# Optimization experiments

Hardware: AMD Instinct MI355X
Metric: run time of the kernel (lower is better)

## Reference

```python
import jax, jax.numpy as jnp
import numpy as np

EMA_OLD = 0.01  # original: m[z] = m[z]*0.01 + y*0.99
EMA_NEW = 0.99

def setup_inputs() -> dict:
    key = jax.random.key(0)
    k1, k2, k3, k4 = jax.random.split(key, 4)
    B, n, C, L = 4096, 1024, 64, 64
    y = jax.random.normal(k1, (B, C, L), dtype=jnp.float32)   # encoder latents
    m = jax.random.normal(k2, (n, C, L), dtype=jnp.float32)   # codebook means
    sd = jax.random.uniform(k3, (n, C, L), dtype=jnp.float32) # codebook variances (init ones in orig)
    p = jax.random.uniform(k4, (n,), dtype=jnp.float32)       # cluster counts
    return {"y": y, "m": m, "sd": sd, "p": p}

def reference(y, m, sd, p):
    B, C, L = y.shape
    n = m.shape[0]
    # pairwise squared distances via ||y||^2 - 2 y.m + ||m||^2 (GEMM form)
    yf = y.reshape(B, C * L)
    mf = m.reshape(n, C * L)
    d2 = ((yf * yf).sum(-1, keepdims=True)
          - 2.0 * (yf @ mf.T)
          + (mf * mf).sum(-1)[None, :])            # [B, n]
    z = jnp.argmin(d2, axis=1)                      # [B] assignments
    new_m = m.at[z].set(m[z] * EMA_OLD + y * EMA_NEW)
    # original updates sd using the ALREADY-updated m gathered at z
    mg = new_m[z]
    new_sd = sd.at[z].set((mg - y) ** 2 * EMA_OLD + sd[z] * EMA_NEW)
    return jnp.concatenate([new_m, new_sd], axis=0)  # [2n, C, L]
```

## Files before the change

kernel.cpp:

```cpp
#include <hip/hip_runtime.h>

#define B_ROWS 4096
#define N_CLUST 1024
#define KDIM 4096
#define NKT 32

#define EMA_OLD 0.01f
#define EMA_NEW 0.99f
#define MARGIN 2.0f

typedef unsigned short ushortT;
typedef _Float16 half8 __attribute__((ext_vector_type(8)));
typedef float f32x16 __attribute__((ext_vector_type(16)));

#define WS_WINNER_OFF 0
#define WS_Z_OFF      4096
#define WS_YY_OFF     20480
#define WS_MM_OFF     36864
#define WS_D2A_OFF    65536
#define WS_D2B_OFF    (WS_D2A_OFF + 16777216)
#define WS_YHI_OFF    (WS_D2B_OFF + 16777216)
#define WS_MHI_OFF    (WS_YHI_OFF + 33554432)
#define WS_END        (WS_MHI_OFF + 8388608)

__global__ __launch_bounds__(256) void convert_sumsq(
    const float* __restrict__ ysrc, const float* __restrict__ msrc,
    ushortT* __restrict__ yhi, ushortT* __restrict__ mhi,
    float* __restrict__ yy, float* __restrict__ mm) {
    const int blk = blockIdx.x;
    const float* src;
    ushortT* hi;
    float* out;
    int row;
    if (blk < B_ROWS) {
        src = ysrc; hi = yhi; out = yy + blk; row = blk;
    } else {
        row = blk - B_ROWS;
        src = msrc; hi = mhi; out = mm + row;
    }
    const int r = row & 63, rb = row >> 6;
    const int t = threadIdx.x;
    float s = 0.f;
#pragma unroll
    for (int h = 0; h < 2; ++h) {
        int ci = h * 256 + t;
        int kt = ci >> 4, p = ci & 15;
        int c = p ^ (r & 15);
        const float* sp = src + ((size_t)row << 12) + kt * 128 + c * 8;
        float4 v0 = *(const float4*)sp;
        float4 v1 = *(const float4*)(sp + 4);
        float vv[8] = {v0.x, v0.y, v0.z, v0.w, v1.x, v1.y, v1.z, v1.w};
        half8 hv;
#pragma unroll
        for (int i = 0; i < 8; ++i) {
            hv[i] = (_Float16)vv[i];
            s += vv[i] * vv[i];
        }
        size_t off = (((size_t)rb * NKT + kt) * 64 + r) * 128 + p * 8;
        *(half8*)(hi + off) = hv;
    }
    for (int off = 32; off > 0; off >>= 1) s += __shfl_down(s, off, 64);
    __shared__ float red[4];
    if ((t & 63) == 0) red[t >> 6] = s;
    __syncthreads();
    if (t == 0) out[0] = red[0] + red[1] + red[2] + red[3];
}

__device__ __forceinline__ void gload_lds16(const void* g, void* l) {
    __builtin_amdgcn_global_load_lds(
        (const __attribute__((address_space(1))) unsigned int*)g,
        (__attribute__((address_space(3))) unsigned int*)l, 16, 0, 0);
}

__device__ __forceinline__ half8 ldfrag(const ushortT* s, int r, int c) {
    int p = c ^ (r & 15);
    return *(const half8*)(s + r * 128 + p * 8);
}

__global__ __launch_bounds__(256, 2) void screen_gemm(
    const ushortT* __restrict__ Ah, const ushortT* __restrict__ Bh,
    const float* __restrict__ yy, const float* __restrict__ mm,
    float* __restrict__ d2a, float* __restrict__ d2b) {
    __shared__ __align__(16) ushortT sA[128 * 128];
    __shared__ __align__(16) ushortT sB[128 * 128];

    const int t = threadIdx.x, w = t >> 6, l = t & 63;
    const int by = blockIdx.x & 7;
    const int kh = (blockIdx.x >> 3) & 1;
    const int bx = blockIdx.x >> 4;
    const int row0 = bx * 128, col0 = by * 128;
    const int wr = (w >> 1) * 64, wc = (w & 1) * 64;
    const int m0 = l & 31, hsel = l >> 5;

    const char* gAbase = (const char*)Ah + (size_t)l * 16;
    const char* gBbase = (const char*)Bh + (size_t)l * 16;

    f32x16 acc[2][2];
#pragma unroll
    for (int i = 0; i < 2; ++i)
#pragma unroll
        for (int j = 0; j < 2; ++j)
#pragma unroll
            for (int r = 0; r < 16; ++r) acc[i][j][r] = 0.f;

    const int kt0 = kh * (NKT / 2);
    for (int ktt = 0; ktt < NKT / 2; ++ktt) {
        const int kt = kt0 + ktt;
        __syncthreads();
#pragma unroll
        for (int j = 0; j < 8; ++j) {
            int ch = w * 8 + j;
            int tile = ch >> 4, seg = ch & 15;
            size_t go = ((size_t)((2 * bx + tile) * NKT + kt) << 14) +
                        seg * 1024;
            gload_lds16(gAbase + go, (char*)sA + tile * 16384 + seg * 1024);
            size_t gob = ((size_t)((2 * by + tile) * NKT + kt) << 14) +
                         seg * 1024;
            gload_lds16(gBbase + gob, (char*)sB + tile * 16384 + seg * 1024);
        }
        __syncthreads();

        const ushortT* tA = sA + (wr >> 6) * 8192;
        const ushortT* tB = sB + (wc >> 6) * 8192;
#pragma unroll
        for (int kk = 0; kk < 8; ++kk) {
            int c = kk * 2 + hsel;
            half8 a0 = ldfrag(tA, m0, c);
            half8 a1 = ldfrag(tA, 32 + m0, c);
            half8 b0 = ldfrag(tB, m0, c);
            half8 b1 = ldfrag(tB, 32 + m0, c);
            acc[0][0] = __builtin_amdgcn_mfma_f32_32x32x16_f16(a0, b0, acc[0][0], 0, 0, 0);
            acc[0][1] = __builtin_amdgcn_mfma_f32_32x32x16_f16(a0, b1, acc[0][1], 0, 0, 0);
            acc[1][0] = __builtin_amdgcn_mfma_f32_32x32x16_f16(a1, b0, acc[1][0], 0, 0, 0);
            acc[1][1] = __builtin_amdgcn_mfma_f32_32x32x16_f16(a1, b1, acc[1][1], 0, 0, 0);
        }
    }

    if (kh == 0) {
#pragma unroll
        for (int i = 0; i < 2; ++i)
#pragma unroll
            for (int j = 0; j < 2; ++j) {
                const int gcol = col0 + wc + j * 32 + m0;
                const float mv = mm[gcol];
#pragma unroll
                for (int r = 0; r < 16; ++r) {
                    int ri = (r & 3) + 8 * (r >> 2) + 4 * hsel;
                    int grow = row0 + wr + i * 32 + ri;
                    d2a[(size_t)grow * N_CLUST + gcol] =
                        yy[grow] - 2.0f * acc[i][j][r] + mv;
                }
            }
    } else {
#pragma unroll
        for (int i = 0; i < 2; ++i)
#pragma unroll
            for (int j = 0; j < 2; ++j) {
                const int gcol = col0 + wc + j * 32 + m0;
#pragma unroll
                for (int r = 0; r < 16; ++r) {
                    int ri = (r & 3) + 8 * (r >> 2) + 4 * hsel;
                    int grow = row0 + wr + i * 32 + ri;
                    d2b[(size_t)grow * N_CLUST + gcol] = -2.0f * acc[i][j][r];
                }
            }
    }
}

__global__ __launch_bounds__(256) void rescreen(
    const float* __restrict__ d2a, const float* __restrict__ d2b,
    const float* __restrict__ ysrc, const float* __restrict__ msrc,
    const float* __restrict__ yy, const float* __restrict__ mm,
    int* __restrict__ z) {
    const int row = blockIdx.x * 4 + (threadIdx.x >> 6);
    const int l = threadIdx.x & 63;
    const float* dra = d2a + (size_t)row * N_CLUST;
    const float* drb = d2b + (size_t)row * N_CLUST;

    float v[16];
#pragma unroll
    for (int k = 0; k < 16; ++k) v[k] = dra[l + 64 * k] + drb[l + 64 * k];

    float mn = v[0];
#pragma unroll
    for (int k = 1; k < 16; ++k) mn = fminf(mn, v[k]);
#pragma unroll
    for (int s = 1; s <= 32; s <<= 1) mn = fminf(mn, __shfl_xor(mn, s, 64));
    const float thr = mn + MARGIN;

    int cnt = 0;
#pragma unroll
    for (int k = 0; k < 16; ++k) cnt += (v[k] <= thr) ? 1 : 0;
#pragma unroll
    for (int s = 1; s <= 32; s <<= 1) cnt += __shfl_xor(cnt, s, 64);

    int zj;
    if (cnt == 1) {
        int cj = 0x7FFFFFFF;
#pragma unroll
        for (int k = 0; k < 16; ++k)
            if (v[k] <= thr) cj = min(cj, l + 64 * k);
#pragma unroll
        for (int s = 1; s <= 32; s <<= 1) cj = min(cj, __shfl_xor(cj, s, 64));
        zj = cj;
    } else {
        double bestd = 1e300;
        int bestj = -1;
        const float4* yp = (const float4*)(ysrc + (size_t)row * KDIM);
        for (int k = 0; k < 16; ++k) {
            unsigned long long mask = __ballot(v[k] <= thr);
            while (mask) {
                int lb = __ffsll((unsigned long long)mask) - 1;
                mask &= mask - 1;
                int j = 64 * k + lb;
                const float4* mp = (const float4*)(msrc + (size_t)j * KDIM);
                double acc = 0.0;
#pragma unroll
                for (int tt = 0; tt < 16; ++tt) {
                    float4 a = yp[l + 64 * tt];
                    float4 b = mp[l + 64 * tt];
                    acc += (double)a.x * b.x + (double)a.y * b.y +
                           (double)a.z * b.z + (double)a.w * b.w;
                }
#pragma unroll
                for (int s = 1; s <= 32; s <<= 1)
                    acc += __shfl_xor(acc, s, 64);
                double d2x = (double)yy[row] - 2.0 * acc + (double)mm[j];
                if (d2x < bestd) { bestd = d2x; bestj = j; }
            }
        }
        zj = bestj;
    }
    if (l == 0) z[row] = zj;
}

__global__ void pick_winner(const int* __restrict__ z,
                            int* __restrict__ winner) {
    int b = blockIdx.x * blockDim.x + threadIdx.x;
    if (b < B_ROWS) atomicMax(&winner[z[b]], b);
}

__global__ __launch_bounds__(256) void write_out(
    const float* __restrict__ y, const float* __restrict__ m,
    const float* __restrict__ sd, const int* __restrict__ winner,
    float* __restrict__ out) {
    const int idx = blockIdx.x;
    const int t = threadIdx.x;
    const int w = winner[idx];
    const float4* mp = (const float4*)(m + (size_t)idx * KDIM);
    const float4* sp = (const float4*)(sd + (size_t)idx * KDIM);
    float4* om = (float4*)(out + (size_t)idx * KDIM);
    float4* os = (float4*)(out + (size_t)(N_CLUST + idx) * KDIM);
    if (w >= 0) {
        const float4* yp = (const float4*)(y + (size_t)w * KDIM);
        for (int i = t; i < KDIM / 4; i += 256) {
            float4 mv = mp[i], yv = yp[i], sv = sp[i];
            float4 nm, ns;
            nm.x = mv.x * EMA_OLD + yv.x * EMA_NEW;
            nm.y = mv.y * EMA_OLD + yv.y * EMA_NEW;
            nm.z = mv.z * EMA_OLD + yv.z * EMA_NEW;
            nm.w = mv.w * EMA_OLD + yv.w * EMA_NEW;
            float dx = nm.x - yv.x, dy = nm.y - yv.y;
            float dz = nm.z - yv.z, dw = nm.w - yv.w;
            ns.x = dx * dx * EMA_OLD + sv.x * EMA_NEW;
            ns.y = dy * dy * EMA_OLD + sv.y * EMA_NEW;
            ns.z = dz * dz * EMA_OLD + sv.z * EMA_NEW;
            ns.w = dw * dw * EMA_OLD + sv.w * EMA_NEW;
            om[i] = nm;
            os[i] = ns;
        }
    } else {
        for (int i = t; i < KDIM / 4; i += 256) {
            om[i] = mp[i];
            os[i] = sp[i];
        }
    }
}

extern "C" void kernel_launch(void* const* d_in, const int* in_sizes, int n_in,
                              void* d_out, int out_size, void* d_ws,
                              size_t ws_size, hipStream_t stream) {
    const float* y  = (const float*)d_in[0];
    const float* m  = (const float*)d_in[1];
    const float* sd = (const float*)d_in[2];
    float* out = (float*)d_out;

    char* ws = (char*)d_ws;
    int* winner = (int*)(ws + WS_WINNER_OFF);
    int* z      = (int*)(ws + WS_Z_OFF);
    float* yy   = (float*)(ws + WS_YY_OFF);
    float* mm   = (float*)(ws + WS_MM_OFF);
    float* d2a  = (float*)(ws + WS_D2A_OFF);
    float* d2b  = (float*)(ws + WS_D2B_OFF);
    ushortT* yhi = (ushortT*)(ws + WS_YHI_OFF);
    ushortT* mhi = (ushortT*)(ws + WS_MHI_OFF);

    hipMemsetAsync(winner, 0xFF, 4096, stream);

    convert_sumsq<<<B_ROWS + N_CLUST, 256, 0, stream>>>(y, m, yhi, mhi, yy, mm);

    screen_gemm<<<(B_ROWS / 128) * (N_CLUST / 128) * 2, 256, 0, stream>>>(
        yhi, mhi, yy, mm, d2a, d2b);

    rescreen<<<B_ROWS / 4, 256, 0, stream>>>(d2a, d2b, y, m, yy, mm, z);

    pick_winner<<<B_ROWS / 256, 256, 0, stream>>>(z, winner);
    write_out<<<N_CLUST, 256, 0, stream>>>(y, m, sd, winner, out);
}
```

Baseline: 216.3 us.

## Double-buffer screen GEMM with half-width K tiles and async LDS prefetch

Splits each 128-wide K tile into two 64-wide halves and double-buffers them in LDS. The next stage is prefetched with global_load_lds while the current stage runs MFMA, using s_waitcnt vmcnt and raw barriers in place of two __syncthreads per tile. It also raises wave priority around the MFMA block. LDS footprint stays the same, but there are twice as many loop iterations and barriers, and correctness depends on the manual vmcnt count and the new swizzle and lane offsets.

Result: slower. 222.6 us (+2.9%).

```diff
diff --git a/kernel.cpp b/kernel.cpp
--- a/kernel.cpp
+++ b/kernel.cpp
@@ -4,6 +4,7 @@
 #define N_CLUST 1024
 #define KDIM 4096
 #define NKT 32
+#define NSTEP 32
 
 #define EMA_OLD 0.01f
 #define EMA_NEW 0.99f
@@ -72,17 +73,17 @@
         (__attribute__((address_space(3))) unsigned int*)l, 16, 0, 0);
 }
 
-__device__ __forceinline__ half8 ldfrag(const ushortT* s, int r, int c) {
-    int p = c ^ (r & 15);
-    return *(const half8*)(s + r * 128 + p * 8);
+__device__ __forceinline__ half8 ldfrag64(const ushortT* s, int r, int c) {
+    int p = c ^ (r & 7);
+    return *(const half8*)(s + r * 64 + p * 8);
 }
 
 __global__ __launch_bounds__(256, 2) void screen_gemm(
     const ushortT* __restrict__ Ah, const ushortT* __restrict__ Bh,
     const float* __restrict__ yy, const float* __restrict__ mm,
     float* __restrict__ d2a, float* __restrict__ d2b) {
-    __shared__ __align__(16) ushortT sA[128 * 128];
-    __shared__ __align__(16) ushortT sB[128 * 128];
+    __shared__ __align__(16) ushortT sA[2][128 * 64];
+    __shared__ __align__(16) ushortT sB[2][128 * 64];
 
     const int t = threadIdx.x, w = t >> 6, l = t & 63;
     const int by = blockIdx.x & 7;
@@ -92,8 +93,9 @@
     const int wr = (w >> 1) * 64, wc = (w & 1) * 64;
     const int m0 = l & 31, hsel = l >> 5;
 
-    const char* gAbase = (const char*)Ah + (size_t)l * 16;
-    const char* gBbase = (const char*)Bh + (size_t)l * 16;
+    const int laneoff = (l >> 3) * 256 + (l & 7) * 16;
+    const char* gAbase = (const char*)Ah + laneoff;
+    const char* gBbase = (const char*)Bh + laneoff;
 
     f32x16 acc[2][2];
 #pragma unroll
@@ -103,38 +105,55 @@
 #pragma unroll
             for (int r = 0; r < 16; ++r) acc[i][j][r] = 0.f;
 
-    const int kt0 = kh * (NKT / 2);
-    for (int ktt = 0; ktt < NKT / 2; ++ktt) {
-        const int kt = kt0 + ktt;
-        __syncthreads();
-#pragma unroll
-        for (int j = 0; j < 8; ++j) {
-            int ch = w * 8 + j;
-            int tile = ch >> 4, seg = ch & 15;
-            size_t go = ((size_t)((2 * bx + tile) * NKT + kt) << 14) +
-                        seg * 1024;
-            gload_lds16(gAbase + go, (char*)sA + tile * 16384 + seg * 1024);
-            size_t gob = ((size_t)((2 * by + tile) * NKT + kt) << 14) +
-                         seg * 1024;
-            gload_lds16(gBbase + gob, (char*)sB + tile * 16384 + seg * 1024);
-        }
-        __syncthreads();
-
-        const ushortT* tA = sA + (wr >> 6) * 8192;
-        const ushortT* tB = sB + (wc >> 6) * 8192;
-#pragma unroll
-        for (int kk = 0; kk < 8; ++kk) {
+#define STAGE(buf, kt2)                                                       \
+    {                                                                         \
+        const int kt_ = (kt2) >> 1, ks_ = (kt2) & 1;                          \
+        _Pragma("unroll")                                                     \
+        for (int j = 0; j < 4; ++j) {                                         \
+            const int g = w * 4 + j;                                          \
+            const int hi_ = (ks_ ^ (g & 1)) << 7;                             \
+            size_t goA = ((size_t)((2 * bx + (g >> 3)) * NKT + kt_) << 14) +  \
+                         (g & 7) * 2048 + hi_;                                \
+            gload_lds16(gAbase + goA, (char*)&sA[buf][0] + g * 1024);         \
+            size_t goB = ((size_t)((2 * by + (g >> 3)) * NKT + kt_) << 14) +  \
+                         (g & 7) * 2048 + hi_;                                \
+            gload_lds16(gBbase + goB, (char*)&sB[buf][0] + g * 1024);         \
+        }                                                                     \
+    }
+
+    const int kt2_0 = kh * NSTEP;
+    STAGE(0, kt2_0);
+
+    for (int i = 0; i < NSTEP; ++i) {
+        const int buf = i & 1;
+        if (i + 1 < NSTEP) {
+            STAGE(buf ^ 1, kt2_0 + i + 1);
+            asm volatile("s_waitcnt vmcnt(8)" ::: "memory");
+        } else {
+            asm volatile("s_waitcnt vmcnt(0)" ::: "memory");
+        }
+        __builtin_amdgcn_s_barrier();
+
+        const ushortT* tA = &sA[buf][0] + wr * 64;
+        const ushortT* tB = &sB[buf][0] + wc * 64;
+        __builtin_amdgcn_s_setprio(1);
+#pragma unroll
+        for (int kk = 0; kk < 4; ++kk) {
             int c = kk * 2 + hsel;
-            half8 a0 = ldfrag(tA, m0, c);
-            half8 a1 = ldfrag(tA, 32 + m0, c);
-            half8 b0 = ldfrag(tB, m0, c);
-            half8 b1 = ldfrag(tB, 32 + m0, c);
+            half8 a0 = ldfrag64(tA, m0, c);
+            half8 a1 = ldfrag64(tA, 32 + m0, c);
+            half8 b0 = ldfrag64(tB, m0, c);
+            half8 b1 = ldfrag64(tB, 32 + m0, c);
             acc[0][0] = __builtin_amdgcn_mfma_f32_32x32x16_f16(a0, b0, acc[0][0], 0, 0, 0);
             acc[0][1] = __builtin_amdgcn_mfma_f32_32x32x16_f16(a0, b1, acc[0][1], 0, 0, 0);
             acc[1][0] = __builtin_amdgcn_mfma_f32_32x32x16_f16(a1, b0, acc[1][0], 0, 0, 0);
             acc[1][1] = __builtin_amdgcn_mfma_f32_32x32x16_f16(a1, b1, acc[1][1], 0, 0, 0);
         }
-    }
+        __builtin_amdgcn_s_setprio(0);
+        asm volatile("" ::: "memory");
+        __builtin_amdgcn_s_barrier();
+    }
+#undef STAGE
 
     if (kh == 0) {
 #pragma unroll
```
